# Kernel tuning notes

Measured on AMD Instinct MI355X. Metric: run time of the kernel, lower is better.

The kernel has to match this reference:

```python
import jax, jax.numpy as jnp
import numpy as np

N, F_IN, F_OUT = 8192, 256, 128
ALPHA = 0.2  # LeakyReLU negative slope
NEG_BIG = -9e15


def setup_inputs() -> dict:
    key = jax.random.key(0)
    k1, k2, k3, k4 = jax.random.split(key, 4)
    h = jax.random.normal(k1, (N, F_IN), dtype=jnp.float32)
    adj = jax.random.randint(k2, (N, N), 0, 2, dtype=jnp.int32)
    # Xavier-uniform-ish scaled params (gain 1.414)
    w_bound = 1.414 * np.sqrt(6.0 / (F_IN + F_OUT))
    a_bound = 1.414 * np.sqrt(6.0 / (2 * F_OUT + 1))
    W = jax.random.uniform(k3, (F_IN, F_OUT), jnp.float32, -w_bound, w_bound)
    a = jax.random.uniform(k4, (2 * F_OUT, 1), jnp.float32, -a_bound, a_bound)
    return {"h": h, "adj": adj, "W": W, "a": a}


def reference(h, adj, W, a):
    # Wh: [N, F_OUT]
    Wh = h @ W
    # a = [a1; a2]; e_ij = leakyrelu(a1.Wh_i + a2.Wh_j) == the torch concat+matmul,
    # computed via broadcast-add instead of materializing [N, N, 2F].
    a1 = a[:F_OUT, 0]   # [F_OUT]
    a2 = a[F_OUT:, 0]   # [F_OUT]
    si = Wh @ a1        # [N]
    sj = Wh @ a2        # [N]
    e = jax.nn.leaky_relu(si[:, None] + sj[None, :], negative_slope=ALPHA)  # [N, N]
    logits = jnp.where(adj > 0, e, NEG_BIG)
    attention = jax.nn.softmax(logits, axis=1)
    # dropout is identity in eval mode (training=False)
    h_prime = attention @ Wh  # [N, F_OUT]
    return jax.nn.elu(h_prime)  # concat=True path
```

## Files before the change

### kernel.cpp

```cpp
#include <hip/hip_runtime.h>

#define NN 8192
#define FIN 256
#define FOUT 128
#define BKJ 128
#define JSPLIT 4
#define LALPHA 0.2f
#define NEGB -9.0e15f
#define LOG2E 1.4426950408889634f

typedef short bf16x8 __attribute__((ext_vector_type(8)));
typedef float f32x4 __attribute__((ext_vector_type(4)));

#define FOR8(X) X(0) X(1) X(2) X(3) X(4) X(5) X(6) X(7)

static __device__ __forceinline__ unsigned short f2bf(float f) {
    unsigned u = __float_as_uint(f);
    u += 0x7FFFu + ((u >> 16) & 1u);
    return (unsigned short)(u >> 16);
}
static __device__ __forceinline__ float ex2(float x) {
    float r; asm("v_exp_f32 %0, %1" : "=v"(r) : "v"(x)); return r;
}
static __device__ __forceinline__ int cvtpk(float lo, float hi) {
    int r; asm("v_cvt_pk_bf16_f32 %0, %1, %2" : "=v"(r) : "v"(lo), "v"(hi)); return r;
}

__global__ __launch_bounds__(256) void gat_k1(
    const float* __restrict__ h, const float* __restrict__ W,
    const float* __restrict__ a, unsigned short* __restrict__ WhT,
    float* __restrict__ si, float* __restrict__ sj, float* __restrict__ sjl)
{
    __shared__ float Wt[64 * 128];
    __shared__ float hT[64 * 36 + 4];
    const int t = threadIdx.x;
    const int r0 = blockIdx.x * 32;
    const int rg = t >> 5;
    const int cg = t & 31;
    float acc[4][4] = {{0.f,0.f,0.f,0.f},{0.f,0.f,0.f,0.f},{0.f,0.f,0.f,0.f},{0.f,0.f,0.f,0.f}};

    for (int kc = 0; kc < 4; ++kc) {
        __syncthreads();
        const float4* Ws = (const float4*)(W + kc * 64 * FOUT);
        float4* Wd = (float4*)Wt;
        #pragma unroll
        for (int v = 0; v < 8; ++v) Wd[v * 256 + t] = Ws[v * 256 + t];
        {
            const int hr = t >> 3, hk = (t & 7) * 8;
            const float* hs = h + (size_t)(r0 + hr) * FIN + kc * 64 + hk;
            float4 x0 = *(const float4*)hs;
            float4 x1 = *(const float4*)(hs + 4);
            hT[(hk + 0) * 36 + hr] = x0.x; hT[(hk + 1) * 36 + hr] = x0.y;
            hT[(hk + 2) * 36 + hr] = x0.z; hT[(hk + 3) * 36 + hr] = x0.w;
            hT[(hk + 4) * 36 + hr] = x1.x; hT[(hk + 5) * 36 + hr] = x1.y;
            hT[(hk + 6) * 36 + hr] = x1.z; hT[(hk + 7) * 36 + hr] = x1.w;
        }
        __syncthreads();
        #pragma unroll 8
        for (int kk = 0; kk < 64; ++kk) {
            float4 hv4 = *(const float4*)&hT[kk * 36 + rg * 4];
            float4 wv4 = *(const float4*)&Wt[kk * 128 + cg * 4];
            float hv[4] = {hv4.x, hv4.y, hv4.z, hv4.w};
            float wv[4] = {wv4.x, wv4.y, wv4.z, wv4.w};
            #pragma unroll
            for (int rr = 0; rr < 4; ++rr)
                #pragma unroll
                for (int cc = 0; cc < 4; ++cc)
                    acc[rr][cc] = fmaf(hv[rr], wv[cc], acc[rr][cc]);
        }
    }
    float4 a1v4 = *(const float4*)(a + cg * 4);
    float4 a2v4 = *(const float4*)(a + FOUT + cg * 4);
    float a1v[4] = {a1v4.x, a1v4.y, a1v4.z, a1v4.w};
    float a2v[4] = {a2v4.x, a2v4.y, a2v4.z, a2v4.w};
    float ps[4], qs[4];
    #pragma unroll
    for (int rr = 0; rr < 4; ++rr) {
        float p = 0.f, q = 0.f;
        #pragma unroll
        for (int cc = 0; cc < 4; ++cc) {
            p = fmaf(acc[rr][cc], a1v[cc], p);
            q = fmaf(acc[rr][cc], a2v[cc], q);
        }
        ps[rr] = p; qs[rr] = q;
    }
    #pragma unroll
    for (int off = 1; off <= 16; off <<= 1) {
        #pragma unroll
        for (int rr = 0; rr < 4; ++rr) {
            ps[rr] += __shfl_xor(ps[rr], off);
            qs[rr] += __shfl_xor(qs[rr], off);
        }
    }
    if (cg == 0) {
        #pragma unroll
        for (int rr = 0; rr < 4; ++rr) {
            si[r0 + rg * 4 + rr] = ps[rr];
            sj[r0 + rg * 4 + rr] = qs[rr];
            sjl[r0 + rg * 4 + rr] = qs[rr] * LOG2E;
        }
    }
    #pragma unroll
    for (int cc = 0; cc < 4; ++cc) {
        ushort4 v;
        v.x = f2bf(acc[0][cc]); v.y = f2bf(acc[1][cc]);
        v.z = f2bf(acc[2][cc]); v.w = f2bf(acc[3][cc]);
        *(ushort4*)(WhT + (size_t)(cg * 4 + cc) * NN + r0 + rg * 4) = v;
    }
}

__global__ __launch_bounds__(256) void gat_k1s(
    const float* __restrict__ sj, float* __restrict__ sjmax)
{
    __shared__ float red[256];
    float m = -1e30f;
    for (int i = threadIdx.x; i < NN; i += 256) m = fmaxf(m, sj[i]);
    red[threadIdx.x] = m;
    __syncthreads();
    for (int o = 128; o > 0; o >>= 1) {
        if (threadIdx.x < o) red[threadIdx.x] = fmaxf(red[threadIdx.x], red[threadIdx.x + o]);
        __syncthreads();
    }
    if (threadIdx.x == 0) sjmax[0] = red[0];
}

static __device__ __forceinline__ float pe(int av, float sjlv, float a2, float b2) {
    float t1 = a2 + sjlv;
    float t2 = fmaf(0.2f, sjlv, b2);
    float y = fmaxf(t1, t2);
    y = (av > 0) ? y : NEGB;
    return ex2(y);
}

template<int JS, bool FINAL>
__global__ __launch_bounds__(256, 2) void gat_k2(
    const int* __restrict__ adj, const unsigned short* __restrict__ WhT,
    const float* __restrict__ si, const float* __restrict__ sjl,
    const float* __restrict__ sjmaxp,
    float* __restrict__ lsum, float* __restrict__ Opart, float* __restrict__ out)
{
    const int JR_ = NN / JS;
    const int NST_ = JR_ / BKJ;
    __shared__ __align__(16) unsigned short tile[2][16384];
    const int t = threadIdx.x;
    const int w = t >> 6, l = t & 63;
    const int rb = (int)blockIdx.x / JS, js = (int)blockIdx.x % JS;
    const int iw = rb * 64 + w * 16;
    const int j0 = js * JR_;
    const int row = l & 15, kg = l >> 4;

    const float si_l = si[iw + row];
    const float sjmax = sjmaxp[0];
    const float xm = si_l + sjmax;
    const float m_row = fmaxf(xm, LALPHA * xm);
    const float a2 = (si_l - m_row) * LOG2E;
    const float b2 = (LALPHA * si_l - m_row) * LOG2E;
    const float* sjb = sjl + j0 + kg * 8;
    const int* adjb = adj + (size_t)(iw + row) * NN + j0 + kg * 8;

#define GSRC_D(v) const unsigned short* gsrc##v = WhT + (size_t)(v * 16 + (t >> 4)) * NN + j0 + (t & 15) * 8; \
                  const int ldo##v = ((v * 256 + t) * 16) ^ (((t >> 4) & 7) << 4);
    FOR8(GSRC_D)

#define REG_D(v) int4 stg##v, adr##v;
    FOR8(REG_D)
#define STG_L0(v) stg##v = *(const int4*)(gsrc##v);
    FOR8(STG_L0)
#define ADR_L0(q) adr##q = *(const int4*)(adjb + (q / 2) * 32 + (q % 2) * 4);
    FOR8(ADR_L0)

#define ACC_D(n) f32x4 acc##n = {0.f, 0.f, 0.f, 0.f};
    FOR8(ACC_D)
    f32x4 acc8 = {0.f, 0.f, 0.f, 0.f};
    bf16x8 ones;
    #pragma unroll
    for (int z = 0; z < 8; ++z) ones[z] = (short)0x3F80;
    const int kg16 = kg * 16;

#define STG_WR(v) *(int4*)((char*)tb + ldo##v) = stg##v;
#define STG_LN(v) stg##v = *(const int4*)(gsrc##v + so);
#define ADR_LN(q) adr##q = *(const int4*)(adjb + so + (q / 2) * 32 + (q % 2) * 4);
#define P8(AF, A0, A1, sp) { \
    float4 s0_ = *(const float4*)(sp); float4 s1_ = *(const float4*)((sp) + 4); \
    float p0_ = pe(A0.x, s0_.x, a2, b2), p1_ = pe(A0.y, s0_.y, a2, b2); \
    float p2_ = pe(A0.z, s0_.z, a2, b2), p3_ = pe(A0.w, s0_.w, a2, b2); \
    float p4_ = pe(A1.x, s1_.x, a2, b2), p5_ = pe(A1.y, s1_.y, a2, b2); \
    float p6_ = pe(A1.z, s1_.z, a2, b2), p7_ = pe(A1.w, s1_.w, a2, b2); \
    int4 w_; w_.x = cvtpk(p0_, p1_); w_.y = cvtpk(p2_, p3_); \
    w_.z = cvtpk(p4_, p5_); w_.w = cvtpk(p6_, p7_); \
    AF = __builtin_bit_cast(bf16x8, w_); }
#define MFMA_ROW(n) { const int c_ = n * 16 + row; \
    const int off_ = c_ * 256 + ((KB ^ ((c_ & 7) << 4))); \
    bf16x8 bv_ = *(const bf16x8*)((const char*)tb + off_); \
    acc##n = __builtin_amdgcn_mfma_f32_16x16x32_bf16(AFk, bv_, acc##n, 0, 0, 0); }
#define MFMA_KC(afv, kcl) { const bf16x8 AFk = afv; const int KB = kcl * 64 + kg16; FOR8(MFMA_ROW) \
    acc8 = __builtin_amdgcn_mfma_f32_16x16x32_bf16(AFk, ones, acc8, 0, 0, 0); }

    for (int s = 0; s < NST_; ++s) {
        unsigned short* tb = tile[s & 1];
        bf16x8 af0, af1, af2, af3;
        {
            const float* spp = sjb + s * BKJ;
            P8(af0, adr0, adr1, spp)
            P8(af1, adr2, adr3, spp + 32)
            P8(af2, adr4, adr5, spp + 64)
            P8(af3, adr6, adr7, spp + 96)
        }
        if (s + 1 < NST_) {
            const size_t so = (size_t)(s + 1) * BKJ;
            FOR8(ADR_LN)
        }
        FOR8(STG_WR)
        if (s + 1 < NST_) {
            const size_t so = (size_t)(s + 1) * BKJ;
            FOR8(STG_LN)
        }
        __builtin_amdgcn_sched_barrier(0);
        asm volatile("s_waitcnt lgkmcnt(0)" ::: "memory");
        __builtin_amdgcn_s_barrier();
        __builtin_amdgcn_sched_barrier(0);
        MFMA_KC(af0, 0) MFMA_KC(af1, 1) MFMA_KC(af2, 2) MFMA_KC(af3, 3)
    }

    if (FINAL) {
#define FN_ROW(n) { size_t ob = (size_t)(iw + kg * 4) * FOUT + n * 16 + row; \
    float o0 = acc##n[0] / acc8[0]; out[ob]            = (o0 > 0.f) ? o0 : expm1f(o0); \
    float o1 = acc##n[1] / acc8[1]; out[ob + FOUT]     = (o1 > 0.f) ? o1 : expm1f(o1); \
    float o2 = acc##n[2] / acc8[2]; out[ob + 2 * FOUT] = (o2 > 0.f) ? o2 : expm1f(o2); \
    float o3 = acc##n[3] / acc8[3]; out[ob + 3 * FOUT] = (o3 > 0.f) ? o3 : expm1f(o3); }
        FOR8(FN_ROW)
    } else {
        if (row == 0) {
            #pragma unroll
            for (int q = 0; q < 4; ++q)
                lsum[(size_t)js * NN + iw + kg * 4 + q] = acc8[q];
        }
#define ST_ROW(n) { size_t ob = ((size_t)js * NN + iw + kg * 4) * FOUT + n * 16 + row; \
    Opart[ob] = acc##n[0]; Opart[ob + FOUT] = acc##n[1]; \
    Opart[ob + 2 * FOUT] = acc##n[2]; Opart[ob + 3 * FOUT] = acc##n[3]; }
        FOR8(ST_ROW)
    }
}

__global__ __launch_bounds__(256) void gat_k3(
    const float* __restrict__ lsum, const float* __restrict__ Opart,
    float* __restrict__ out)
{
    const int t = threadIdx.x;
    const int i = (int)blockIdx.x * 2 + (t >> 7);
    const int f = t & 127;
    float den = 0.f, num = 0.f;
    const size_t SP = (size_t)NN * FOUT;
    size_t base = (size_t)i * FOUT + f;
    #pragma unroll
    for (int k = 0; k < JSPLIT; ++k) {
        den += lsum[(size_t)k * NN + i];
        num += Opart[(size_t)k * SP + base];
    }
    float o = num / den;
    out[base] = (o > 0.f) ? o : expm1f(o);
}

extern "C" void kernel_launch(void* const* d_in, const int* in_sizes, int n_in,
                              void* d_out, int out_size, void* d_ws, size_t ws_size,
                              hipStream_t stream) {
    const float* h  = (const float*)d_in[0];
    const int*  adj = (const int*)d_in[1];
    const float* W  = (const float*)d_in[2];
    const float* a  = (const float*)d_in[3];
    float* out = (float*)d_out;
    char* ws = (char*)d_ws;
    unsigned short* WhT = (unsigned short*)ws;
    float* si     = (float*)(ws + 2097152);
    float* sj     = (float*)(ws + 2129920);
    float* sjl    = (float*)(ws + 2162688);
    float* sjmax  = (float*)(ws + 2195456);
    float* lsum   = (float*)(ws + 2195712);
    float* Opart  = (float*)(ws + 2326784);
    const size_t need = 2326784 + (size_t)JSPLIT * NN * FOUT * 4;

    gat_k1<<<256, 256, 0, stream>>>(h, W, a, WhT, si, sj, sjl);
    gat_k1s<<<1, 256, 0, stream>>>(sj, sjmax);
    if (ws_size >= need) {
        gat_k2<JSPLIT, false><<<128 * JSPLIT, 256, 0, stream>>>(adj, WhT, si, sjl, sjmax, lsum, Opart, out);
        gat_k3<<<4096, 256, 0, stream>>>(lsum, Opart, out);
    } else {
        gat_k2<1, true><<<128, 256, 0, stream>>>(adj, WhT, si, sjl, sjmax, lsum, Opart, out);
    }
}
```

Measured before the change: 98.02 us.

## Pre-pack adjacency into bitmask before attention kernel

Result: slower. 113.9 us (+16.1%).

```diff
diff --git a/kernel.cpp b/kernel.cpp
--- a/kernel.cpp
+++ b/kernel.cpp
@@ -124,17 +124,40 @@
     if (threadIdx.x == 0) sjmax[0] = red[0];
 }
 
-static __device__ __forceinline__ float pe(int av, float sjlv, float a2, float b2) {
+__global__ __launch_bounds__(256) void gat_pack(
+    const int* __restrict__ adj, unsigned long long* __restrict__ mask)
+{
+    const int lane = threadIdx.x & 63;
+    const int wv = ((int)blockIdx.x * 4) + (threadIdx.x >> 6);
+    const int NW = 2048 * 4;
+    const int NCH = NN * NN / 64;
+    for (int base = wv * 4; base < NCH; base += NW * 4) {
+        int v0 = adj[(size_t)(base + 0) * 64 + lane];
+        int v1 = adj[(size_t)(base + 1) * 64 + lane];
+        int v2 = adj[(size_t)(base + 2) * 64 + lane];
+        int v3 = adj[(size_t)(base + 3) * 64 + lane];
+        unsigned long long m0 = __ballot(v0 > 0);
+        unsigned long long m1 = __ballot(v1 > 0);
+        unsigned long long m2 = __ballot(v2 > 0);
+        unsigned long long m3 = __ballot(v3 > 0);
+        if (lane < 4) {
+            unsigned long long m = (lane == 0) ? m0 : (lane == 1) ? m1 : (lane == 2) ? m2 : m3;
+            mask[base + lane] = m;
+        }
+    }
+}
+
+static __device__ __forceinline__ float pe(unsigned bit, float sjlv, float a2, float b2) {
     float t1 = a2 + sjlv;
     float t2 = fmaf(0.2f, sjlv, b2);
     float y = fmaxf(t1, t2);
-    y = (av > 0) ? y : NEGB;
+    y = bit ? y : NEGB;
     return ex2(y);
 }
 
 template<int JS, bool FINAL>
 __global__ __launch_bounds__(256, 2) void gat_k2(
-    const int* __restrict__ adj, const unsigned short* __restrict__ WhT,
+    const unsigned int* __restrict__ maskdw, const unsigned short* __restrict__ WhT,
     const float* __restrict__ si, const float* __restrict__ sjl,
     const float* __restrict__ sjmaxp,
     float* __restrict__ lsum, float* __restrict__ Opart, float* __restrict__ out)
@@ -148,6 +171,7 @@
     const int iw = rb * 64 + w * 16;
     const int j0 = js * JR_;
     const int row = l & 15, kg = l >> 4;
+    const int kg8 = kg * 8;
 
     const float si_l = si[iw + row];
     const float sjmax = sjmaxp[0];
@@ -155,19 +179,18 @@
     const float m_row = fmaxf(xm, LALPHA * xm);
     const float a2 = (si_l - m_row) * LOG2E;
     const float b2 = (LALPHA * si_l - m_row) * LOG2E;
-    const float* sjb = sjl + j0 + kg * 8;
-    const int* adjb = adj + (size_t)(iw + row) * NN + j0 + kg * 8;
+    const float* sjb = sjl + j0 + kg8;
+    const unsigned int* mrow = maskdw + (size_t)(iw + row) * (NN / 32) + (j0 >> 5);
 
 #define GSRC_D(v) const unsigned short* gsrc##v = WhT + (size_t)(v * 16 + (t >> 4)) * NN + j0 + (t & 15) * 8; \
                   const int ldo##v = ((v * 256 + t) * 16) ^ (((t >> 4) & 7) << 4);
     FOR8(GSRC_D)
 
-#define REG_D(v) int4 stg##v, adr##v;
+#define REG_D(v) int4 stg##v;
     FOR8(REG_D)
 #define STG_L0(v) stg##v = *(const int4*)(gsrc##v);
     FOR8(STG_L0)
-#define ADR_L0(q) adr##q = *(const int4*)(adjb + (q / 2) * 32 + (q % 2) * 4);
-    FOR8(ADR_L0)
+    uint4 mi = *(const uint4*)mrow;
 
 #define ACC_D(n) f32x4 acc##n = {0.f, 0.f, 0.f, 0.f};
     FOR8(ACC_D)
@@ -179,13 +202,13 @@
 
 #define STG_WR(v) *(int4*)((char*)tb + ldo##v) = stg##v;
 #define STG_LN(v) stg##v = *(const int4*)(gsrc##v + so);
-#define ADR_LN(q) adr##q = *(const int4*)(adjb + so + (q / 2) * 32 + (q % 2) * 4);
-#define P8(AF, A0, A1, sp) { \
+#define P8(AF, MW, sp) { \
     float4 s0_ = *(const float4*)(sp); float4 s1_ = *(const float4*)((sp) + 4); \
-    float p0_ = pe(A0.x, s0_.x, a2, b2), p1_ = pe(A0.y, s0_.y, a2, b2); \
-    float p2_ = pe(A0.z, s0_.z, a2, b2), p3_ = pe(A0.w, s0_.w, a2, b2); \
-    float p4_ = pe(A1.x, s1_.x, a2, b2), p5_ = pe(A1.y, s1_.y, a2, b2); \
-    float p6_ = pe(A1.z, s1_.z, a2, b2), p7_ = pe(A1.w, s1_.w, a2, b2); \
+    const unsigned sh_ = (MW) >> kg8; \
+    float p0_ = pe((sh_ >> 0) & 1u, s0_.x, a2, b2), p1_ = pe((sh_ >> 1) & 1u, s0_.y, a2, b2); \
+    float p2_ = pe((sh_ >> 2) & 1u, s0_.z, a2, b2), p3_ = pe((sh_ >> 3) & 1u, s0_.w, a2, b2); \
+    float p4_ = pe((sh_ >> 4) & 1u, s1_.x, a2, b2), p5_ = pe((sh_ >> 5) & 1u, s1_.y, a2, b2); \
+    float p6_ = pe((sh_ >> 6) & 1u, s1_.z, a2, b2), p7_ = pe((sh_ >> 7) & 1u, s1_.w, a2, b2); \
     int4 w_; w_.x = cvtpk(p0_, p1_); w_.y = cvtpk(p2_, p3_); \
     w_.z = cvtpk(p4_, p5_); w_.w = cvtpk(p6_, p7_); \
     AF = __builtin_bit_cast(bf16x8, w_); }
@@ -201,15 +224,12 @@
         bf16x8 af0, af1, af2, af3;
         {
             const float* spp = sjb + s * BKJ;
-            P8(af0, adr0, adr1, spp)
-            P8(af1, adr2, adr3, spp + 32)
-            P8(af2, adr4, adr5, spp + 64)
-            P8(af3, adr6, adr7, spp + 96)
-        }
-        if (s + 1 < NST_) {
-            const size_t so = (size_t)(s + 1) * BKJ;
-            FOR8(ADR_LN)
-        }
+            P8(af0, mi.x, spp)
+            P8(af1, mi.y, spp + 32)
+            P8(af2, mi.z, spp + 64)
+            P8(af3, mi.w, spp + 96)
+        }
+        if (s + 1 < NST_) mi = *(const uint4*)(mrow + (s + 1) * 4);
         FOR8(STG_WR)
         if (s + 1 < NST_) {
             const size_t so = (size_t)(s + 1) * BKJ;
@@ -276,15 +296,19 @@
     float* sjl    = (float*)(ws + 2162688);
     float* sjmax  = (float*)(ws + 2195456);
     float* lsum   = (float*)(ws + 2195712);
-    float* Opart  = (float*)(ws + 2326784);
-    const size_t need = 2326784 + (size_t)JSPLIT * NN * FOUT * 4;
+    unsigned long long* mask = (unsigned long long*)(ws + 2326784);
+    float* Opart  = (float*)(ws + 10715392);
+    const size_t need = 10715392 + (size_t)JSPLIT * NN * FOUT * 4;
 
     gat_k1<<<256, 256, 0, stream>>>(h, W, a, WhT, si, sj, sjl);
     gat_k1s<<<1, 256, 0, stream>>>(sj, sjmax);
+    gat_pack<<<2048, 256, 0, stream>>>(adj, mask);
     if (ws_size >= need) {
-        gat_k2<JSPLIT, false><<<128 * JSPLIT, 256, 0, stream>>>(adj, WhT, si, sjl, sjmax, lsum, Opart, out);
+        gat_k2<JSPLIT, false><<<128 * JSPLIT, 256, 0, stream>>>(
+            (const unsigned int*)mask, WhT, si, sjl, sjmax, lsum, Opart, out);
         gat_k3<<<4096, 256, 0, stream>>>(lsum, Opart, out);
     } else {
-        gat_k2<1, true><<<128, 256, 0, stream>>>(adj, WhT, si, sjl, sjmax, lsum, Opart, out);
-    }
-}
+        gat_k2<1, true><<<128, 256, 0, stream>>>(
+            (const unsigned int*)mask, WhT, si, sjl, sjmax, lsum, Opart, out);
+    }
+}
```

## Process two 16-row groups per wave to reuse WhT tile, stage sj in LDS

Applied to the files above, without the earlier changes.

Result: slower. 101.6 us (+3.6%).

```diff
diff --git a/kernel.cpp b/kernel.cpp
--- a/kernel.cpp
+++ b/kernel.cpp
@@ -4,7 +4,7 @@
 #define FIN 256
 #define FOUT 128
 #define BKJ 128
-#define JSPLIT 4
+#define JSPLIT 8
 #define LALPHA 0.2f
 #define NEGB -9.0e15f
 #define LOG2E 1.4426950408889634f
@@ -142,69 +142,87 @@
     const int JR_ = NN / JS;
     const int NST_ = JR_ / BKJ;
     __shared__ __align__(16) unsigned short tile[2][16384];
+    __shared__ __align__(16) float sjl_lds[NN / JS];
     const int t = threadIdx.x;
     const int w = t >> 6, l = t & 63;
     const int rb = (int)blockIdx.x / JS, js = (int)blockIdx.x % JS;
-    const int iw = rb * 64 + w * 16;
+    const int iw0 = rb * 128 + w * 32;
+    const int iw1 = iw0 + 16;
     const int j0 = js * JR_;
     const int row = l & 15, kg = l >> 4;
-
-    const float si_l = si[iw + row];
+    const int kg8 = kg * 8;
+
     const float sjmax = sjmaxp[0];
-    const float xm = si_l + sjmax;
-    const float m_row = fmaxf(xm, LALPHA * xm);
-    const float a2 = (si_l - m_row) * LOG2E;
-    const float b2 = (LALPHA * si_l - m_row) * LOG2E;
-    const float* sjb = sjl + j0 + kg * 8;
-    const int* adjb = adj + (size_t)(iw + row) * NN + j0 + kg * 8;
+    const float si_l0 = si[iw0 + row];
+    const float si_l1 = si[iw1 + row];
+    const float xm0 = si_l0 + sjmax, xm1 = si_l1 + sjmax;
+    const float m0 = fmaxf(xm0, LALPHA * xm0), m1 = fmaxf(xm1, LALPHA * xm1);
+    const float a2A = (si_l0 - m0) * LOG2E, b2A = (LALPHA * si_l0 - m0) * LOG2E;
+    const float a2B = (si_l1 - m1) * LOG2E, b2B = (LALPHA * si_l1 - m1) * LOG2E;
+    const int* adjb0 = adj + (size_t)(iw0 + row) * NN + j0 + kg8;
+    const int* adjb1 = adj + (size_t)(iw1 + row) * NN + j0 + kg8;
+
+    for (int i = t * 4; i < JR_; i += 1024)
+        *(float4*)&sjl_lds[i] = *(const float4*)(sjl + j0 + i);
 
 #define GSRC_D(v) const unsigned short* gsrc##v = WhT + (size_t)(v * 16 + (t >> 4)) * NN + j0 + (t & 15) * 8; \
                   const int ldo##v = ((v * 256 + t) * 16) ^ (((t >> 4) & 7) << 4);
     FOR8(GSRC_D)
 
-#define REG_D(v) int4 stg##v, adr##v;
+#define REG_D(v) int4 stg##v, adrA##v, adrB##v;
     FOR8(REG_D)
 #define STG_L0(v) stg##v = *(const int4*)(gsrc##v);
     FOR8(STG_L0)
-#define ADR_L0(q) adr##q = *(const int4*)(adjb + (q / 2) * 32 + (q % 2) * 4);
+#define ADR_L0(q) adrA##q = *(const int4*)(adjb0 + (q / 2) * 32 + (q % 2) * 4); \
+                  adrB##q = *(const int4*)(adjb1 + (q / 2) * 32 + (q % 2) * 4);
     FOR8(ADR_L0)
 
-#define ACC_D(n) f32x4 acc##n = {0.f, 0.f, 0.f, 0.f};
+#define ACC_D(n) f32x4 accA##n = {0.f, 0.f, 0.f, 0.f}; f32x4 accB##n = {0.f, 0.f, 0.f, 0.f};
     FOR8(ACC_D)
-    f32x4 acc8 = {0.f, 0.f, 0.f, 0.f};
+    f32x4 acc8A = {0.f, 0.f, 0.f, 0.f};
+    f32x4 acc8B = {0.f, 0.f, 0.f, 0.f};
     bf16x8 ones;
     #pragma unroll
     for (int z = 0; z < 8; ++z) ones[z] = (short)0x3F80;
     const int kg16 = kg * 16;
 
+    __syncthreads();
+
 #define STG_WR(v) *(int4*)((char*)tb + ldo##v) = stg##v;
 #define STG_LN(v) stg##v = *(const int4*)(gsrc##v + so);
-#define ADR_LN(q) adr##q = *(const int4*)(adjb + so + (q / 2) * 32 + (q % 2) * 4);
-#define P8(AF, A0, A1, sp) { \
-    float4 s0_ = *(const float4*)(sp); float4 s1_ = *(const float4*)((sp) + 4); \
-    float p0_ = pe(A0.x, s0_.x, a2, b2), p1_ = pe(A0.y, s0_.y, a2, b2); \
-    float p2_ = pe(A0.z, s0_.z, a2, b2), p3_ = pe(A0.w, s0_.w, a2, b2); \
-    float p4_ = pe(A1.x, s1_.x, a2, b2), p5_ = pe(A1.y, s1_.y, a2, b2); \
-    float p6_ = pe(A1.z, s1_.z, a2, b2), p7_ = pe(A1.w, s1_.w, a2, b2); \
+#define ADR_LN(q) adrA##q = *(const int4*)(adjb0 + so + (q / 2) * 32 + (q % 2) * 4); \
+                  adrB##q = *(const int4*)(adjb1 + so + (q / 2) * 32 + (q % 2) * 4);
+#define P8(AF, A0, A1, off, A2C, B2C) { \
+    float4 s0_ = *(const float4*)&sjl_lds[(off)]; float4 s1_ = *(const float4*)&sjl_lds[(off) + 4]; \
+    float p0_ = pe(A0.x, s0_.x, A2C, B2C), p1_ = pe(A0.y, s0_.y, A2C, B2C); \
+    float p2_ = pe(A0.z, s0_.z, A2C, B2C), p3_ = pe(A0.w, s0_.w, A2C, B2C); \
+    float p4_ = pe(A1.x, s1_.x, A2C, B2C), p5_ = pe(A1.y, s1_.y, A2C, B2C); \
+    float p6_ = pe(A1.z, s1_.z, A2C, B2C), p7_ = pe(A1.w, s1_.w, A2C, B2C); \
     int4 w_; w_.x = cvtpk(p0_, p1_); w_.y = cvtpk(p2_, p3_); \
     w_.z = cvtpk(p4_, p5_); w_.w = cvtpk(p6_, p7_); \
     AF = __builtin_bit_cast(bf16x8, w_); }
-#define MFMA_ROW(n) { const int c_ = n * 16 + row; \
+#define MFMA_N(n) { const int c_ = n * 16 + row; \
     const int off_ = c_ * 256 + ((KB ^ ((c_ & 7) << 4))); \
     bf16x8 bv_ = *(const bf16x8*)((const char*)tb + off_); \
-    acc##n = __builtin_amdgcn_mfma_f32_16x16x32_bf16(AFk, bv_, acc##n, 0, 0, 0); }
-#define MFMA_KC(afv, kcl) { const bf16x8 AFk = afv; const int KB = kcl * 64 + kg16; FOR8(MFMA_ROW) \
-    acc8 = __builtin_amdgcn_mfma_f32_16x16x32_bf16(AFk, ones, acc8, 0, 0, 0); }
+    accA##n = __builtin_amdgcn_mfma_f32_16x16x32_bf16(AFa, bv_, accA##n, 0, 0, 0); \
+    accB##n = __builtin_amdgcn_mfma_f32_16x16x32_bf16(AFb, bv_, accB##n, 0, 0, 0); }
+#define MFMA_KC2(afa, afb, kcl) { const bf16x8 AFa = afa, AFb = afb; const int KB = kcl * 64 + kg16; FOR8(MFMA_N) \
+    acc8A = __builtin_amdgcn_mfma_f32_16x16x32_bf16(AFa, ones, acc8A, 0, 0, 0); \
+    acc8B = __builtin_amdgcn_mfma_f32_16x16x32_bf16(AFb, ones, acc8B, 0, 0, 0); }
 
     for (int s = 0; s < NST_; ++s) {
         unsigned short* tb = tile[s & 1];
-        bf16x8 af0, af1, af2, af3;
+        bf16x8 afA0, afA1, afA2, afA3, afB0, afB1, afB2, afB3;
         {
-            const float* spp = sjb + s * BKJ;
-            P8(af0, adr0, adr1, spp)
-            P8(af1, adr2, adr3, spp + 32)
-            P8(af2, adr4, adr5, spp + 64)
-            P8(af3, adr6, adr7, spp + 96)
+            const int off = s * BKJ + kg8;
+            P8(afA0, adrA0, adrA1, off,      a2A, b2A)
+            P8(afA1, adrA2, adrA3, off + 32, a2A, b2A)
+            P8(afA2, adrA4, adrA5, off + 64, a2A, b2A)
+            P8(afA3, adrA6, adrA7, off + 96, a2A, b2A)
+            P8(afB0, adrB0, adrB1, off,      a2B, b2B)
+            P8(afB1, adrB2, adrB3, off + 32, a2B, b2B)
+            P8(afB2, adrB4, adrB5, off + 64, a2B, b2B)
+            P8(afB3, adrB6, adrB7, off + 96, a2B, b2B)
         }
         if (s + 1 < NST_) {
             const size_t so = (size_t)(s + 1) * BKJ;
@@ -219,25 +237,32 @@
         asm volatile("s_waitcnt lgkmcnt(0)" ::: "memory");
         __builtin_amdgcn_s_barrier();
         __builtin_amdgcn_sched_barrier(0);
-        MFMA_KC(af0, 0) MFMA_KC(af1, 1) MFMA_KC(af2, 2) MFMA_KC(af3, 3)
+        MFMA_KC2(afA0, afB0, 0) MFMA_KC2(afA1, afB1, 1)
+        MFMA_KC2(afA2, afB2, 2) MFMA_KC2(afA3, afB3, 3)
     }
 
     if (FINAL) {
-#define FN_ROW(n) { size_t ob = (size_t)(iw + kg * 4) * FOUT + n * 16 + row; \
-    float o0 = acc##n[0] / acc8[0]; out[ob]            = (o0 > 0.f) ? o0 : expm1f(o0); \
-    float o1 = acc##n[1] / acc8[1]; out[ob + FOUT]     = (o1 > 0.f) ? o1 : expm1f(o1); \
-    float o2 = acc##n[2] / acc8[2]; out[ob + 2 * FOUT] = (o2 > 0.f) ? o2 : expm1f(o2); \
-    float o3 = acc##n[3] / acc8[3]; out[ob + 3 * FOUT] = (o3 > 0.f) ? o3 : expm1f(o3); }
+#define FN_ROW(n) { \
+    size_t obA = (size_t)(iw0 + kg * 4) * FOUT + n * 16 + row; \
+    size_t obB = (size_t)(iw1 + kg * 4) * FOUT + n * 16 + row; \
+    _Pragma("unroll") for (int r = 0; r < 4; ++r) { \
+        float oA = accA##n[r] / acc8A[r]; out[obA + (size_t)r * FOUT] = (oA > 0.f) ? oA : expm1f(oA); \
+        float oB = accB##n[r] / acc8B[r]; out[obB + (size_t)r * FOUT] = (oB > 0.f) ? oB : expm1f(oB); } }
         FOR8(FN_ROW)
     } else {
         if (row == 0) {
             #pragma unroll
-            for (int q = 0; q < 4; ++q)
-                lsum[(size_t)js * NN + iw + kg * 4 + q] = acc8[q];
-        }
-#define ST_ROW(n) { size_t ob = ((size_t)js * NN + iw + kg * 4) * FOUT + n * 16 + row; \
-    Opart[ob] = acc##n[0]; Opart[ob + FOUT] = acc##n[1]; \
-    Opart[ob + 2 * FOUT] = acc##n[2]; Opart[ob + 3 * FOUT] = acc##n[3]; }
+            for (int q = 0; q < 4; ++q) {
+                lsum[(size_t)js * NN + iw0 + kg * 4 + q] = acc8A[q];
+                lsum[(size_t)js * NN + iw1 + kg * 4 + q] = acc8B[q];
+            }
+        }
+#define ST_ROW(n) { \
+    size_t obA = ((size_t)js * NN + iw0 + kg * 4) * FOUT + n * 16 + row; \
+    size_t obB = ((size_t)js * NN + iw1 + kg * 4) * FOUT + n * 16 + row; \
+    _Pragma("unroll") for (int r = 0; r < 4; ++r) { \
+        Opart[obA + (size_t)r * FOUT] = accA##n[r]; \
+        Opart[obB + (size_t)r * FOUT] = accB##n[r]; } }
         FOR8(ST_ROW)
     }
 }
@@ -276,15 +301,15 @@
     float* sjl    = (float*)(ws + 2162688);
     float* sjmax  = (float*)(ws + 2195456);
     float* lsum   = (float*)(ws + 2195712);
-    float* Opart  = (float*)(ws + 2326784);
-    const size_t need = 2326784 + (size_t)JSPLIT * NN * FOUT * 4;
+    float* Opart  = (float*)(ws + 2457856);
+    const size_t need = 2457856 + (size_t)JSPLIT * NN * FOUT * 4;
 
     gat_k1<<<256, 256, 0, stream>>>(h, W, a, WhT, si, sj, sjl);
     gat_k1s<<<1, 256, 0, stream>>>(sj, sjmax);
     if (ws_size >= need) {
-        gat_k2<JSPLIT, false><<<128 * JSPLIT, 256, 0, stream>>>(adj, WhT, si, sjl, sjmax, lsum, Opart, out);
+        gat_k2<JSPLIT, false><<<64 * JSPLIT, 256, 0, stream>>>(adj, WhT, si, sjl, sjmax, lsum, Opart, out);
         gat_k3<<<4096, 256, 0, stream>>>(lsum, Opart, out);
     } else {
-        gat_k2<1, true><<<128, 256, 0, stream>>>(adj, WhT, si, sjl, sjmax, lsum, Opart, out);
-    }
-}
+        gat_k2<1, true><<<64, 256, 0, stream>>>(adj, WhT, si, sjl, sjmax, lsum, Opart, out);
+    }
+}
```

## Factor LeakyReLU exponent into per-column tables and split positive/negative MFMA accumulators

Applied to the files above, without the earlier changes.

Measured after the change: 105.0 us. +7.2%, slower.

```diff
diff --git a/kernel.cpp b/kernel.cpp
--- a/kernel.cpp
+++ b/kernel.cpp
@@ -6,7 +6,6 @@
 #define BKJ 128
 #define JSPLIT 4
 #define LALPHA 0.2f
-#define NEGB -9.0e15f
 #define LOG2E 1.4426950408889634f
 
 typedef short bf16x8 __attribute__((ext_vector_type(8)));
@@ -22,14 +21,11 @@
 static __device__ __forceinline__ float ex2(float x) {
     float r; asm("v_exp_f32 %0, %1" : "=v"(r) : "v"(x)); return r;
 }
-static __device__ __forceinline__ int cvtpk(float lo, float hi) {
-    int r; asm("v_cvt_pk_bf16_f32 %0, %1, %2" : "=v"(r) : "v"(lo), "v"(hi)); return r;
-}
 
 __global__ __launch_bounds__(256) void gat_k1(
     const float* __restrict__ h, const float* __restrict__ W,
     const float* __restrict__ a, unsigned short* __restrict__ WhT,
-    float* __restrict__ si, float* __restrict__ sj, float* __restrict__ sjl)
+    float* __restrict__ si, float* __restrict__ sj)
 {
     __shared__ float Wt[64 * 128];
     __shared__ float hT[64 * 36 + 4];
@@ -97,7 +93,6 @@
         for (int rr = 0; rr < 4; ++rr) {
             si[r0 + rg * 4 + rr] = ps[rr];
             sj[r0 + rg * 4 + rr] = qs[rr];
-            sjl[r0 + rg * 4 + rr] = qs[rr] * LOG2E;
         }
     }
     #pragma unroll
@@ -109,8 +104,9 @@
     }
 }
 
-__global__ __launch_bounds__(256) void gat_k1s(
-    const float* __restrict__ sj, float* __restrict__ sjmax)
+__global__ __launch_bounds__(256) void gat_k1v(
+    const float* __restrict__ sj, float* __restrict__ sjmax,
+    unsigned short* __restrict__ vpk, unsigned short* __restrict__ zpk)
 {
     __shared__ float red[256];
     float m = -1e30f;
@@ -122,41 +118,48 @@
         __syncthreads();
     }
     if (threadIdx.x == 0) sjmax[0] = red[0];
-}
-
-static __device__ __forceinline__ float pe(int av, float sjlv, float a2, float b2) {
-    float t1 = a2 + sjlv;
-    float t2 = fmaf(0.2f, sjlv, b2);
-    float y = fmaxf(t1, t2);
-    y = (av > 0) ? y : NEGB;
-    return ex2(y);
+    __syncthreads();
+    const float mx = red[0];
+    for (int i = threadIdx.x; i < NN; i += 256) {
+        float d = sj[i] - mx;
+        vpk[i] = f2bf(ex2(d * LOG2E));
+        zpk[i] = f2bf(ex2(LALPHA * d * LOG2E));
+    }
 }
 
 template<int JS, bool FINAL>
 __global__ __launch_bounds__(256, 2) void gat_k2(
     const int* __restrict__ adj, const unsigned short* __restrict__ WhT,
-    const float* __restrict__ si, const float* __restrict__ sjl,
-    const float* __restrict__ sjmaxp,
+    const float* __restrict__ si, const unsigned short* __restrict__ vpk,
+    const unsigned short* __restrict__ zpk, const float* __restrict__ sjmaxp,
     float* __restrict__ lsum, float* __restrict__ Opart, float* __restrict__ out)
 {
     const int JR_ = NN / JS;
     const int NST_ = JR_ / BKJ;
     __shared__ __align__(16) unsigned short tile[2][16384];
+    __shared__ __align__(16) unsigned short vpk_lds[NN / JS];
+    __shared__ __align__(16) unsigned short zpk_lds[NN / JS];
     const int t = threadIdx.x;
     const int w = t >> 6, l = t & 63;
     const int rb = (int)blockIdx.x / JS, js = (int)blockIdx.x % JS;
     const int iw = rb * 64 + w * 16;
     const int j0 = js * JR_;
     const int row = l & 15, kg = l >> 4;
+    const int kg8 = kg * 8;
 
     const float si_l = si[iw + row];
     const float sjmax = sjmaxp[0];
     const float xm = si_l + sjmax;
     const float m_row = fmaxf(xm, LALPHA * xm);
-    const float a2 = (si_l - m_row) * LOG2E;
-    const float b2 = (LALPHA * si_l - m_row) * LOG2E;
-    const float* sjb = sjl + j0 + kg * 8;
-    const int* adjb = adj + (size_t)(iw + row) * NN + j0 + kg * 8;
+    const float thr = ex2(-xm * LOG2E);
+    const float uu = ex2((xm - m_row) * LOG2E);
+    const float ww = ex2((LALPHA * xm - m_row) * LOG2E);
+    const int* adjb = adj + (size_t)(iw + row) * NN + j0 + kg8;
+
+    for (int i = t * 8; i < JR_; i += 2048) {
+        *(int4*)&vpk_lds[i] = *(const int4*)(vpk + j0 + i);
+        *(int4*)&zpk_lds[i] = *(const int4*)(zpk + j0 + i);
+    }
 
 #define GSRC_D(v) const unsigned short* gsrc##v = WhT + (size_t)(v * 16 + (t >> 4)) * NN + j0 + (t & 15) * 8; \
                   const int ldo##v = ((v * 256 + t) * 16) ^ (((t >> 4) & 7) << 4);
@@ -169,42 +172,59 @@
 #define ADR_L0(q) adr##q = *(const int4*)(adjb + (q / 2) * 32 + (q % 2) * 4);
     FOR8(ADR_L0)
 
-#define ACC_D(n) f32x4 acc##n = {0.f, 0.f, 0.f, 0.f};
+#define ACC_D(n) f32x4 accP##n = {0.f, 0.f, 0.f, 0.f}; f32x4 accN##n = {0.f, 0.f, 0.f, 0.f};
     FOR8(ACC_D)
-    f32x4 acc8 = {0.f, 0.f, 0.f, 0.f};
+    f32x4 acc8P = {0.f, 0.f, 0.f, 0.f};
+    f32x4 acc8N = {0.f, 0.f, 0.f, 0.f};
     bf16x8 ones;
     #pragma unroll
     for (int z = 0; z < 8; ++z) ones[z] = (short)0x3F80;
     const int kg16 = kg * 16;
+
+    __syncthreads();
 
 #define STG_WR(v) *(int4*)((char*)tb + ldo##v) = stg##v;
 #define STG_LN(v) stg##v = *(const int4*)(gsrc##v + so);
 #define ADR_LN(q) adr##q = *(const int4*)(adjb + so + (q / 2) * 32 + (q % 2) * 4);
-#define P8(AF, A0, A1, sp) { \
-    float4 s0_ = *(const float4*)(sp); float4 s1_ = *(const float4*)((sp) + 4); \
-    float p0_ = pe(A0.x, s0_.x, a2, b2), p1_ = pe(A0.y, s0_.y, a2, b2); \
-    float p2_ = pe(A0.z, s0_.z, a2, b2), p3_ = pe(A0.w, s0_.w, a2, b2); \
-    float p4_ = pe(A1.x, s1_.x, a2, b2), p5_ = pe(A1.y, s1_.y, a2, b2); \
-    float p6_ = pe(A1.z, s1_.z, a2, b2), p7_ = pe(A1.w, s1_.w, a2, b2); \
-    int4 w_; w_.x = cvtpk(p0_, p1_); w_.y = cvtpk(p2_, p3_); \
-    w_.z = cvtpk(p4_, p5_); w_.w = cvtpk(p6_, p7_); \
-    AF = __builtin_bit_cast(bf16x8, w_); }
-#define MFMA_ROW(n) { const int c_ = n * 16 + row; \
+#define PAIR(idx, av0, av1, vw, zw) { \
+    const unsigned vw_ = (unsigned)(vw), zw_ = (unsigned)(zw); \
+    const unsigned vh_ = vw_ & 0xFFFF0000u; \
+    const float v0f = __uint_as_float(vw_ << 16); \
+    const float v1f = __uint_as_float(vh_); \
+    const bool m0 = (av0) > 0, m1 = (av1) > 0; \
+    const bool b0 = v0f > thr, b1 = v1f > thr; \
+    pw[idx] = (int)(((m0 && b0) ? (vw_ & 0xFFFFu) : 0u) | ((m1 && b1) ? vh_ : 0u)); \
+    nw[idx] = (int)(((m0 && !b0) ? (zw_ & 0xFFFFu) : 0u) | ((m1 && !b1) ? (zw_ & 0xFFFF0000u) : 0u)); }
+#define P8S(AFP, AFN, A0, A1, voff) { \
+    int4 VP = *(const int4*)&vpk_lds[(voff)]; \
+    int4 ZP = *(const int4*)&zpk_lds[(voff)]; \
+    int pw[4], nw[4]; \
+    PAIR(0, A0.x, A0.y, VP.x, ZP.x) \
+    PAIR(1, A0.z, A0.w, VP.y, ZP.y) \
+    PAIR(2, A1.x, A1.y, VP.z, ZP.z) \
+    PAIR(3, A1.z, A1.w, VP.w, ZP.w) \
+    int4 pi = {pw[0], pw[1], pw[2], pw[3]}; \
+    int4 ni = {nw[0], nw[1], nw[2], nw[3]}; \
+    AFP = __builtin_bit_cast(bf16x8, pi); \
+    AFN = __builtin_bit_cast(bf16x8, ni); }
+#define MFMA_ROW2(n) { const int c_ = n * 16 + row; \
     const int off_ = c_ * 256 + ((KB ^ ((c_ & 7) << 4))); \
     bf16x8 bv_ = *(const bf16x8*)((const char*)tb + off_); \
-    acc##n = __builtin_amdgcn_mfma_f32_16x16x32_bf16(AFk, bv_, acc##n, 0, 0, 0); }
-#define MFMA_KC(afv, kcl) { const bf16x8 AFk = afv; const int KB = kcl * 64 + kg16; FOR8(MFMA_ROW) \
-    acc8 = __builtin_amdgcn_mfma_f32_16x16x32_bf16(AFk, ones, acc8, 0, 0, 0); }
+    accP##n = __builtin_amdgcn_mfma_f32_16x16x32_bf16(AP, bv_, accP##n, 0, 0, 0); \
+    accN##n = __builtin_amdgcn_mfma_f32_16x16x32_bf16(AN, bv_, accN##n, 0, 0, 0); }
+#define MFMA_KC2(afp, afn, kcl) { const bf16x8 AP = afp, AN = afn; const int KB = kcl * 64 + kg16; FOR8(MFMA_ROW2) \
+    acc8P = __builtin_amdgcn_mfma_f32_16x16x32_bf16(AP, ones, acc8P, 0, 0, 0); \
+    acc8N = __builtin_amdgcn_mfma_f32_16x16x32_bf16(AN, ones, acc8N, 0, 0, 0); }
 
     for (int s = 0; s < NST_; ++s) {
         unsigned short* tb = tile[s & 1];
-        bf16x8 af0, af1, af2, af3;
+        bf16x8 afP0, afP1, afP2, afP3, afN0, afN1, afN2, afN3;
         {
-            const float* spp = sjb + s * BKJ;
-            P8(af0, adr0, adr1, spp)
-            P8(af1, adr2, adr3, spp + 32)
-            P8(af2, adr4, adr5, spp + 64)
-            P8(af3, adr6, adr7, spp + 96)
+            const int off = s * BKJ + kg8;
+            P8S(afP0, afN0, adr0, adr1, off)
+            P8S(afP1, afN1, adr2, adr3, off + 32)
+            P8S(afP2, afN2, adr4, adr5, off + 64)
+            P8S(afP3, afN3, adr6, adr7, off + 96)
         }
         if (s + 1 < NST_) {
             const size_t so = (size_t)(s + 1) * BKJ;
@@ -219,25 +239,35 @@
         asm volatile("s_waitcnt lgkmcnt(0)" ::: "memory");
         __builtin_amdgcn_s_barrier();
         __builtin_amdgcn_sched_barrier(0);
-        MFMA_KC(af0, 0) MFMA_KC(af1, 1) MFMA_KC(af2, 2) MFMA_KC(af3, 3)
-    }
+        MFMA_KC2(afP0, afN0, 0) MFMA_KC2(afP1, afN1, 1)
+        MFMA_KC2(afP2, afN2, 2) MFMA_KC2(afP3, afN3, 3)
+    }
+
+    float uq[4], wq[4];
+    #pragma unroll
+    for (int r = 0; r < 4; ++r) {
+        uq[r] = __shfl(uu, kg * 4 + r);
+        wq[r] = __shfl(ww, kg * 4 + r);
+    }
+    float den[4];
+    #pragma unroll
+    for (int r = 0; r < 4; ++r) den[r] = uq[r] * acc8P[r] + wq[r] * acc8N[r];
 
     if (FINAL) {
 #define FN_ROW(n) { size_t ob = (size_t)(iw + kg * 4) * FOUT + n * 16 + row; \
-    float o0 = acc##n[0] / acc8[0]; out[ob]            = (o0 > 0.f) ? o0 : expm1f(o0); \
-    float o1 = acc##n[1] / acc8[1]; out[ob + FOUT]     = (o1 > 0.f) ? o1 : expm1f(o1); \
-    float o2 = acc##n[2] / acc8[2]; out[ob + 2 * FOUT] = (o2 > 0.f) ? o2 : expm1f(o2); \
-    float o3 = acc##n[3] / acc8[3]; out[ob + 3 * FOUT] = (o3 > 0.f) ? o3 : expm1f(o3); }
+    _Pragma("unroll") for (int r = 0; r < 4; ++r) { \
+        float o = (uq[r] * accP##n[r] + wq[r] * accN##n[r]) / den[r]; \
+        out[ob + (size_t)r * FOUT] = (o > 0.f) ? o : expm1f(o); } }
         FOR8(FN_ROW)
     } else {
         if (row == 0) {
             #pragma unroll
             for (int q = 0; q < 4; ++q)
-                lsum[(size_t)js * NN + iw + kg * 4 + q] = acc8[q];
+                lsum[(size_t)js * NN + iw + kg * 4 + q] = den[q];
         }
 #define ST_ROW(n) { size_t ob = ((size_t)js * NN + iw + kg * 4) * FOUT + n * 16 + row; \
-    Opart[ob] = acc##n[0]; Opart[ob + FOUT] = acc##n[1]; \
-    Opart[ob + 2 * FOUT] = acc##n[2]; Opart[ob + 3 * FOUT] = acc##n[3]; }
+    _Pragma("unroll") for (int r = 0; r < 4; ++r) \
+        Opart[ob + (size_t)r * FOUT] = uq[r] * accP##n[r] + wq[r] * accN##n[r]; }
         FOR8(ST_ROW)
     }
 }
@@ -273,18 +303,14 @@
     unsigned short* WhT = (unsigned short*)ws;
     float* si     = (float*)(ws + 2097152);
     float* sj     = (float*)(ws + 2129920);
-    float* sjl    = (float*)(ws + 2162688);
-    float* sjmax  = (float*)(ws + 2195456);
+    float* sjmax  = (float*)(ws + 2162688);
+    unsigned short* vpk = (unsigned short*)(ws + 2162944);
+    unsigned short* zpk = (unsigned short*)(ws + 2179328);
     float* lsum   = (float*)(ws + 2195712);
     float* Opart  = (float*)(ws + 2326784);
-    const size_t need = 2326784 + (size_t)JSPLIT * NN * FOUT * 4;
-
-    gat_k1<<<256, 256, 0, stream>>>(h, W, a, WhT, si, sj, sjl);
-    gat_k1s<<<1, 256, 0, stream>>>(sj, sjmax);
-    if (ws_size >= need) {
-        gat_k2<JSPLIT, false><<<128 * JSPLIT, 256, 0, stream>>>(adj, WhT, si, sjl, sjmax, lsum, Opart, out);
-        gat_k3<<<4096, 256, 0, stream>>>(lsum, Opart, out);
-    } else {
-        gat_k2<1, true><<<128, 256, 0, stream>>>(adj, WhT, si, sjl, sjmax, lsum, Opart, out);
-    }
-}
+
+    gat_k1<<<256, 256, 0, stream>>>(h, W, a, WhT, si, sj);
+    gat_k1v<<<1, 256, 0, stream>>>(sj, sjmax, vpk, zpk);
+    gat_k2<JSPLIT, false><<<128 * JSPLIT, 256, 0, stream>>>(adj, WhT, si, vpk, zpk, sjmax, lsum, Opart, out);
+    gat_k3<<<4096, 256, 0, stream>>>(lsum, Opart, out);
+}
```
